# Performance work log

Measured on AMD Instinct MI355X. Metric: run time of the kernel, lower is better.

Reference implementation:

```python
import jax, jax.numpy as jnp
import numpy as np

B, T, D, H = 4, 2048, 1024, 16
HD = D // H  # 64
EPS = 1e-5

def _layernorm(x, g, b):
    mu = jnp.mean(x, axis=-1, keepdims=True)
    var = jnp.var(x, axis=-1, keepdims=True)
    return (x - mu) * jax.lax.rsqrt(var + EPS) * g + b

def setup_inputs() -> dict:
    key = jax.random.key(0)
    ks = jax.random.split(key, 8)
    s = D ** -0.5
    return {
        "x":  jax.random.normal(ks[0], (B, T, D), jnp.float32),
        "Wq": jax.random.normal(ks[1], (H, D, HD), jnp.float32) * s,
        "Wk": jax.random.normal(ks[2], (H, D, HD), jnp.float32) * s,
        "Wv": jax.random.normal(ks[3], (H, D, HD), jnp.float32) * s,
        "Wp": jax.random.normal(ks[4], (D, D), jnp.float32) * s,
        "bp": jnp.zeros((D,), jnp.float32),
        "W1": jax.random.normal(ks[5], (D, 4 * D), jnp.float32) * s,
        "b1": jnp.zeros((4 * D,), jnp.float32),
        "W2": jax.random.normal(ks[6], (4 * D, D), jnp.float32) * (4 * D) ** -0.5,
        "b2": jnp.zeros((D,), jnp.float32),
        "g1": jnp.ones((D,), jnp.float32),
        "be1": jnp.zeros((D,), jnp.float32),
        "g2": jnp.ones((D,), jnp.float32),
        "be2": jnp.zeros((D,), jnp.float32),
    }

def reference(x, Wq, Wk, Wv, Wp, bp, W1, b1, W2, b2, g1, be1, g2, be2):
    # --- pre-LN causal MHA (all heads batched; torch code loops per head) ---
    h = _layernorm(x, g1, be1)                       # [B,T,D]
    q = jnp.einsum('btd,hdk->bhtk', h, Wq)
    k = jnp.einsum('btd,hdk->bhtk', h, Wk)
    v = jnp.einsum('btd,hdk->bhtk', h, Wv)
    scores = jnp.einsum('bhtk,bhsk->bhts', q, k) * (HD ** -0.5)
    causal = jnp.tril(jnp.ones((T, T), bool))
    scores = jnp.where(causal, scores, -jnp.inf)
    w = jax.nn.softmax(scores, axis=-1)              # [B,H,T,T]
    o = jnp.einsum('bhts,bhsk->bhtk', w, v)          # [B,H,T,HD]
    o = o.transpose(0, 2, 1, 3).reshape(x.shape[0], x.shape[1], D)  # concat heads
    x = x + o @ Wp + bp                              # residual 1
    # --- pre-LN FFN ---
    h2 = _layernorm(x, g2, be2)
    ff = jax.nn.relu(h2 @ W1 + b1) @ W2 + b2
    return x + ff
```

## Files before the change

### kernel.cpp

```cpp
#include <hip/hip_runtime.h>
#include <hip/hip_bf16.h>
#include <math.h>

#define Bsz 4
#define Tsz 2048
#define Dsz 1024
#define Hn  16
#define HDs 64

typedef __attribute__((ext_vector_type(8))) short bf16x8;
typedef __attribute__((ext_vector_type(4))) float f32x4;

typedef const __attribute__((address_space(1))) void gvoid;
typedef __attribute__((address_space(3))) void lvoid;

__device__ __forceinline__ void async_copy16(const short* g, short* l) {
    __builtin_amdgcn_global_load_lds((gvoid*)g, (lvoid*)l, 16, 0, 0);
}

__device__ __forceinline__ short f2bf(float x) {
    __hip_bfloat16 h = __float2bfloat16(x);
    return *reinterpret_cast<short*>(&h);
}

__device__ __forceinline__ unsigned int pack_bf16(float hi, float lo) {
    unsigned int uh = __float_as_uint(hi) + 0x8000u;
    unsigned int ul = __float_as_uint(lo) + 0x8000u;
    return __builtin_amdgcn_perm(uh, ul, 0x07060302u);
}

__device__ __forceinline__ size_t headed_idx(int m, int c) {
    int b = m >> 11, t = m & 2047, h = c >> 6, kc = c & 63;
    return (((size_t)(b * Hn + h) * Tsz + t) << 6) + kc;
}

__global__ __launch_bounds__(256) void ln_kernel(const float* __restrict__ x,
                                                 const float* __restrict__ g,
                                                 const float* __restrict__ beta,
                                                 short* __restrict__ out)
{
    const int row = blockIdx.x;
    const float* xr = x + (size_t)row * Dsz;
    float v[4];
    float s = 0.f, s2 = 0.f;
#pragma unroll
    for (int i = 0; i < 4; ++i) {
        v[i] = xr[threadIdx.x + 256 * i];
        s += v[i];
        s2 += v[i] * v[i];
    }
#pragma unroll
    for (int off = 32; off; off >>= 1) {
        s  += __shfl_xor(s,  off);
        s2 += __shfl_xor(s2, off);
    }
    __shared__ float red[8];
    const int wave = threadIdx.x >> 6;
    if ((threadIdx.x & 63) == 0) { red[wave * 2] = s; red[wave * 2 + 1] = s2; }
    __syncthreads();
    s  = red[0] + red[2] + red[4] + red[6];
    s2 = red[1] + red[3] + red[5] + red[7];
    const float mu  = s * (1.f / Dsz);
    const float var = s2 * (1.f / Dsz) - mu * mu;
    const float rs  = rsqrtf(var + 1e-5f);
    short* orow = out + (size_t)row * Dsz;
#pragma unroll
    for (int i = 0; i < 4; ++i) {
        int col = threadIdx.x + 256 * i;
        orow[col] = f2bf((v[i] - mu) * rs * g[col] + beta[col]);
    }
}

__global__ __launch_bounds__(256) void transpose_cvt(
    const float* __restrict__ in, short* __restrict__ outp, int R, int C)
{
    __shared__ float tile[32][33];
    const int r0 = blockIdx.y * 32, c0 = blockIdx.x * 32;
    const size_t so = (size_t)blockIdx.z * R * C;
    const int tx = threadIdx.x & 31, ty = threadIdx.x >> 5;
    const float* ip = in + so;
    short* op = outp + so;
#pragma unroll
    for (int i = 0; i < 4; ++i)
        tile[ty + i * 8][tx] = ip[(size_t)(r0 + ty + i * 8) * C + c0 + tx];
    __syncthreads();
#pragma unroll
    for (int i = 0; i < 4; ++i)
        op[(size_t)(c0 + ty + i * 8) * R + r0 + tx] = f2bf(tile[tx][ty + i * 8]);
}

__global__ __launch_bounds__(256) void transpose_cvt_qkv(
    const float* __restrict__ Wq, const float* __restrict__ Wk,
    const float* __restrict__ Wv, short* __restrict__ outp)
{
    __shared__ float tile[32][33];
    const int z = blockIdx.z;
    const float* in = (z < 16) ? Wq : (z < 32) ? Wk : Wv;
    const int zz = z & 15;
    const int r0 = blockIdx.y * 32, c0 = blockIdx.x * 32;
    const int tx = threadIdx.x & 31, ty = threadIdx.x >> 5;
    const float* ip = in + (size_t)zz * (1024 * 64);
    short* op = outp + (size_t)z * (1024 * 64);
#pragma unroll
    for (int i = 0; i < 4; ++i)
        tile[ty + i * 8][tx] = ip[(size_t)(r0 + ty + i * 8) * 64 + c0 + tx];
    __syncthreads();
#pragma unroll
    for (int i = 0; i < 4; ++i)
        op[(size_t)(c0 + ty + i * 8) * 1024 + r0 + tx] = f2bf(tile[tx][ty + i * 8]);
}

template <int EPI>
__global__ __launch_bounds__(256) void gemm_mfma(
    const short* __restrict__ A, const short* __restrict__ Bt,
    const float* __restrict__ bias, const float* __restrict__ resid,
    float* __restrict__ Cf, short* __restrict__ Cb0,
    short* __restrict__ Cb1, short* __restrict__ Cb2,
    int M, int N, int K, float scale)
{
    __shared__ short As[128 * 32];
    __shared__ short Bs[128 * 32];
    const int tid  = threadIdx.x;
    const int lane = tid & 63, wave = tid >> 6;
    const int quad = lane >> 4, l16 = lane & 15;
    const int m0 = blockIdx.y * 128, n0 = blockIdx.x * 128;
    const int wm = (wave >> 1) * 64, wn = (wave & 1) * 64;

    f32x4 acc[4][4];
#pragma unroll
    for (int i = 0; i < 4; ++i)
#pragma unroll
        for (int j = 0; j < 4; ++j) acc[i][j] = f32x4{0.f, 0.f, 0.f, 0.f};

    const short* gA = A  + (size_t)(m0 + wave * 32 + (lane >> 2)) * K + (lane & 3) * 8;
    const short* gB = Bt + (size_t)(n0 + wave * 32 + (lane >> 2)) * K + (lane & 3) * 8;
    short* lA0 = As + wave * 1024;
    short* lA1 = As + wave * 1024 + 512;
    short* lB0 = Bs + wave * 1024;
    short* lB1 = Bs + wave * 1024 + 512;
    const size_t rstep = (size_t)16 * K;

    for (int k0 = 0; k0 < K; k0 += 32) {
        async_copy16(gA,         lA0);
        async_copy16(gA + rstep, lA1);
        async_copy16(gB,         lB0);
        async_copy16(gB + rstep, lB1);
        gA += 32; gB += 32;
        __syncthreads();
        bf16x8 af[4], bfr[4];
#pragma unroll
        for (int mt = 0; mt < 4; ++mt)
            af[mt] = *(const bf16x8*)(As + (wm + mt * 16 + l16) * 32 + quad * 8);
#pragma unroll
        for (int nt = 0; nt < 4; ++nt)
            bfr[nt] = *(const bf16x8*)(Bs + (wn + nt * 16 + l16) * 32 + quad * 8);
#pragma unroll
        for (int mt = 0; mt < 4; ++mt)
#pragma unroll
            for (int nt = 0; nt < 4; ++nt)
                acc[mt][nt] = __builtin_amdgcn_mfma_f32_16x16x32_bf16(
                    af[mt], bfr[nt], acc[mt][nt], 0, 0, 0);
        __syncthreads();
    }

#pragma unroll
    for (int mt = 0; mt < 4; ++mt) {
#pragma unroll
        for (int nt = 0; nt < 4; ++nt) {
#pragma unroll
            for (int r = 0; r < 4; ++r) {
                const int m = m0 + wm + mt * 16 + quad * 4 + r;
                const int c = n0 + wn + nt * 16 + l16;
                float val = acc[mt][nt][r];
                if (EPI == 0) {
                    const int sel = c >> 10, cl = c & 1023;
                    if (sel == 0)
                        Cb0[headed_idx(m, cl)] = f2bf(val * scale);
                    else if (sel == 1)
                        Cb1[headed_idx(m, cl)] = f2bf(val);
                    else {
                        int b = m >> 11, t = m & 2047;
                        size_t idx = ((((size_t)((b << 4) | (cl >> 6)) << 6) | (cl & 63)) << 11) | t;
                        Cb2[idx] = f2bf(val);
                    }
                } else if (EPI == 2) {
                    size_t idx = (size_t)m * N + c;
                    Cf[idx] = val + bias[c] + resid[idx];
                } else {
                    float v2 = val + bias[c];
                    Cb0[(size_t)m * N + c] = f2bf(v2 > 0.f ? v2 : 0.f);
                }
            }
        }
    }
}

__global__ __launch_bounds__(256) void fattn_kernel(
    const short* __restrict__ Q,
    const short* __restrict__ K,
    const short* __restrict__ VT,
    short* __restrict__ O)
{
    __shared__ short p_lds[4][2][16 * 64];
    const int lane = threadIdx.x & 63;
    const int wave = threadIdx.x >> 6;
    const int quad = lane >> 4;
    const int l16  = lane & 15;
    const int j    = blockIdx.x * 4 + wave;
    const int bb = blockIdx.y >> 4, hh = blockIdx.y & 15;
    const size_t bhoff = (size_t)blockIdx.y * (Tsz * HDs);
    const short* Qb = Q + bhoff;
    const short* Kb = K + bhoff;
    const short* Vb = VT + bhoff;

    short* pw[2] = { &p_lds[wave][0][0], &p_lds[wave][1][0] };
    const int rd0 = l16 * 64 + (((quad    ) ^ (l16 & 7)) << 3);
    const int rd1 = l16 * 64 + (((quad + 4) ^ (l16 & 7)) << 3);

    for (int ti = 0; ti < 2; ++ti) {
        const int q0w = (ti ? (63 - j) : j) * 32;

        bf16x8 bq[2][2];
#pragma unroll
        for (int mt = 0; mt < 2; ++mt) {
            const short* qp = Qb + (size_t)(q0w + mt * 16 + l16) * 64 + quad * 8;
            bq[mt][0] = *(const bf16x8*)qp;
            bq[mt][1] = *(const bf16x8*)(qp + 32);
        }

        f32x4 oaccT[2][4];
        float lacc[2] = {0.f, 0.f};
#pragma unroll
        for (int mt = 0; mt < 2; ++mt)
#pragma unroll
            for (int nt = 0; nt < 4; ++nt) oaccT[mt][nt] = f32x4{0.f, 0.f, 0.f, 0.f};

        const int nch = (q0w + 31) / 64 + 1;

        bf16x8 ak[4][2];
#pragma unroll
        for (int ct = 0; ct < 4; ++ct) {
            const short* kp = Kb + (size_t)(ct * 16 + l16) * 64 + quad * 8;
            ak[ct][0] = *(const bf16x8*)kp;
            ak[ct][1] = *(const bf16x8*)(kp + 32);
        }

        for (int c = 0; c < nch; ++c) {
            const int s0 = c * 64;
            bf16x8 av[4][2];
#pragma unroll
            for (int nt = 0; nt < 4; ++nt) {
                const short* vp = Vb + (size_t)(nt * 16 + l16) * Tsz + s0 + quad * 8;
                av[nt][0] = *(const bf16x8*)vp;
                av[nt][1] = *(const bf16x8*)(vp + 32);
            }
            bf16x8 nk[4][2];
            if (c + 1 < nch) {
#pragma unroll
                for (int ct = 0; ct < 4; ++ct) {
                    const short* kp = Kb + (size_t)(s0 + 64 + ct * 16 + l16) * 64 + quad * 8;
                    nk[ct][0] = *(const bf16x8*)kp;
                    nk[ct][1] = *(const bf16x8*)(kp + 32);
                }
            }
            f32x4 sfr[2][4];
#pragma unroll
            for (int mt = 0; mt < 2; ++mt)
#pragma unroll
                for (int ct = 0; ct < 4; ++ct) {
                    f32x4 cc = {0.f, 0.f, 0.f, 0.f};
                    cc = __builtin_amdgcn_mfma_f32_16x16x32_bf16(ak[ct][0], bq[mt][0], cc, 0, 0, 0);
                    cc = __builtin_amdgcn_mfma_f32_16x16x32_bf16(ak[ct][1], bq[mt][1], cc, 0, 0, 0);
                    sfr[mt][ct] = cc;
                }
            if (s0 + 63 > q0w) {
#pragma unroll
                for (int mt = 0; mt < 2; ++mt) {
                    const int qr = q0w + mt * 16 + l16;
#pragma unroll
                    for (int ct = 0; ct < 4; ++ct)
#pragma unroll
                        for (int r = 0; r < 4; ++r)
                            if (s0 + ct * 16 + quad * 4 + r > qr)
                                sfr[mt][ct][r] = -INFINITY;
                }
            }
#pragma unroll
            for (int mt = 0; mt < 2; ++mt) {
#pragma unroll
                for (int ct = 0; ct < 4; ++ct) {
                    float p0 = __builtin_exp2f(sfr[mt][ct][0]);
                    float p1 = __builtin_exp2f(sfr[mt][ct][1]);
                    float p2 = __builtin_exp2f(sfr[mt][ct][2]);
                    float p3 = __builtin_exp2f(sfr[mt][ct][3]);
                    lacc[mt] += (p0 + p1) + (p2 + p3);
                    uint2 pkv;
                    pkv.x = pack_bf16(p1, p0);
                    pkv.y = pack_bf16(p3, p2);
                    const int g = (2 * ct + (quad >> 1)) ^ (l16 & 7);
                    *(uint2*)(pw[mt] + l16 * 64 + (g << 3) + (quad & 1) * 4) = pkv;
                }
            }
            bf16x8 bp[2][2];
            bp[0][0] = *(const bf16x8*)(pw[0] + rd0);
            bp[0][1] = *(const bf16x8*)(pw[0] + rd1);
            bp[1][0] = *(const bf16x8*)(pw[1] + rd0);
            bp[1][1] = *(const bf16x8*)(pw[1] + rd1);
#pragma unroll
            for (int nt = 0; nt < 4; ++nt)
#pragma unroll
                for (int mt = 0; mt < 2; ++mt) {
                    oaccT[mt][nt] = __builtin_amdgcn_mfma_f32_16x16x32_bf16(av[nt][0], bp[mt][0], oaccT[mt][nt], 0, 0, 0);
                    oaccT[mt][nt] = __builtin_amdgcn_mfma_f32_16x16x32_bf16(av[nt][1], bp[mt][1], oaccT[mt][nt], 0, 0, 0);
                }
            if (c + 1 < nch) {
#pragma unroll
                for (int ct = 0; ct < 4; ++ct) {
                    ak[ct][0] = nk[ct][0];
                    ak[ct][1] = nk[ct][1];
                }
            }
        }
#pragma unroll
        for (int mt = 0; mt < 2; ++mt) {
            float ps = lacc[mt];
            ps += __shfl_xor(ps, 16);
            ps += __shfl_xor(ps, 32);
            const float inv = 1.f / ps;
            short* orow = O + (size_t)(bb * Tsz + q0w + mt * 16 + l16) * Dsz + hh * 64;
#pragma unroll
            for (int nt = 0; nt < 4; ++nt) {
                uint2 pkv;
                pkv.x = pack_bf16(oaccT[mt][nt][1] * inv, oaccT[mt][nt][0] * inv);
                pkv.y = pack_bf16(oaccT[mt][nt][3] * inv, oaccT[mt][nt][2] * inv);
                *(uint2*)(orow + nt * 16 + quad * 4) = pkv;
            }
        }
    }
}

extern "C" void kernel_launch(void* const* d_in, const int* in_sizes, int n_in,
                              void* d_out, int out_size, void* d_ws, size_t ws_size,
                              hipStream_t stream) {
    const float* x   = (const float*)d_in[0];
    const float* Wq  = (const float*)d_in[1];
    const float* Wk  = (const float*)d_in[2];
    const float* Wv  = (const float*)d_in[3];
    const float* Wp  = (const float*)d_in[4];
    const float* bp  = (const float*)d_in[5];
    const float* W1  = (const float*)d_in[6];
    const float* b1  = (const float*)d_in[7];
    const float* W2  = (const float*)d_in[8];
    const float* b2  = (const float*)d_in[9];
    const float* g1  = (const float*)d_in[10];
    const float* be1 = (const float*)d_in[11];
    const float* g2  = (const float*)d_in[12];
    const float* be2 = (const float*)d_in[13];
    float* out = (float*)d_out;
    char*  W   = (char*)d_ws;

    short* h1  = (short*)(W);
    short* ff1 = (short*)(W);
    short* qb  = (short*)(W + (16ull << 20));
    short* kb  = (short*)(W + (32ull << 20));
    short* vtb = (short*)(W + (48ull << 20));
    short* o   = (short*)(W + (64ull << 20));
    short* h2  = (short*)(W + (80ull << 20));
    short* wqt = (short*)(W + (96ull << 20));
    short* wpt = (short*)(W + (102ull << 20));
    short* w1t = (short*)(W + (104ull << 20));
    short* w2t = (short*)(W + (112ull << 20));

    const int M = Bsz * Tsz;
    const float qscale = 0.125f * 1.44269504f;

    transpose_cvt_qkv<<<dim3(2, 32, 48), 256, 0, stream>>>(Wq, Wk, Wv, wqt);
    transpose_cvt<<<dim3(32, 32, 1),  256, 0, stream>>>(Wp, wpt, 1024, 1024);
    transpose_cvt<<<dim3(128, 32, 1), 256, 0, stream>>>(W1, w1t, 1024, 4096);
    transpose_cvt<<<dim3(32, 128, 1), 256, 0, stream>>>(W2, w2t, 4096, 1024);

    ln_kernel<<<dim3(M), 256, 0, stream>>>(x, g1, be1, h1);

    gemm_mfma<0><<<dim3(24, 64), 256, 0, stream>>>(
        h1, wqt, nullptr, nullptr, nullptr, qb, kb, vtb, M, 3072, 1024, qscale);

    fattn_kernel<<<dim3(8, Bsz * Hn), 256, 0, stream>>>(qb, kb, vtb, o);

    gemm_mfma<2><<<dim3(8, 64), 256, 0, stream>>>(
        o, wpt, bp, x, out, nullptr, nullptr, nullptr, M, 1024, 1024, 1.f);

    ln_kernel<<<dim3(M), 256, 0, stream>>>(out, g2, be2, h2);

    gemm_mfma<3><<<dim3(32, 64), 256, 0, stream>>>(
        h2, w1t, b1, nullptr, nullptr, ff1, nullptr, nullptr, M, 4096, 1024, 1.f);

    gemm_mfma<2><<<dim3(8, 64), 256, 0, stream>>>(
        ff1, w2t, b2, out, out, nullptr, nullptr, nullptr, M, 1024, 4096, 1.f);
}
```

Measured before the change: 611.3 us.

## Split attention KV chunks across wave pairs and remap blocks per XCD

The attention grid grows from 8x64 to 32x64 blocks. Each block takes two query tiles, and each tile is handled by two waves that process alternating 64-key chunks. The partial output accumulators and row sums are then combined through LDS. Block indices are also remapped so that all blocks for a given batch-head land on the same XCD, which should improve L2 reuse of K and V. The intent is to shorten the per-wave serial chain and raise occupancy. The cost is extra LDS traffic and two block-wide barriers at the end.

```diff
diff --git a/kernel.cpp b/kernel.cpp
--- a/kernel.cpp
+++ b/kernel.cpp
@@ -202,13 +202,24 @@
     short* __restrict__ O)
 {
     __shared__ short p_lds[4][2][16 * 64];
+    __shared__ float lred[2][2][16];
     const int lane = threadIdx.x & 63;
     const int wave = threadIdx.x >> 6;
     const int quad = lane >> 4;
     const int l16  = lane & 15;
-    const int j    = blockIdx.x * 4 + wave;
-    const int bb = blockIdx.y >> 4, hh = blockIdx.y & 15;
-    const size_t bhoff = (size_t)blockIdx.y * (Tsz * HDs);
+
+    const int lin  = blockIdx.y * 32 + blockIdx.x;
+    const int xcd  = lin & 7;
+    const int slot = lin >> 3;
+    const int bh   = xcd * 8 + (slot >> 5);
+    const int bx   = slot & 31;
+
+    const int tile = (wave < 2) ? (62 - 2 * bx) : (63 - 2 * bx);
+    const int par  = wave & 1;
+    const int q0w  = tile * 32;
+
+    const int bb = bh >> 4, hh = bh & 15;
+    const size_t bhoff = (size_t)bh * (Tsz * HDs);
     const short* Qb = Q + bhoff;
     const short* Kb = K + bhoff;
     const short* Vb = VT + bhoff;
@@ -217,122 +228,144 @@
     const int rd0 = l16 * 64 + (((quad    ) ^ (l16 & 7)) << 3);
     const int rd1 = l16 * 64 + (((quad + 4) ^ (l16 & 7)) << 3);
 
-    for (int ti = 0; ti < 2; ++ti) {
-        const int q0w = (ti ? (63 - j) : j) * 32;
-
-        bf16x8 bq[2][2];
+    bf16x8 bq[2][2];
+#pragma unroll
+    for (int mt = 0; mt < 2; ++mt) {
+        const short* qp = Qb + (size_t)(q0w + mt * 16 + l16) * 64 + quad * 8;
+        bq[mt][0] = *(const bf16x8*)qp;
+        bq[mt][1] = *(const bf16x8*)(qp + 32);
+    }
+
+    f32x4 oaccT[2][4];
+    float lacc[2] = {0.f, 0.f};
+#pragma unroll
+    for (int mt = 0; mt < 2; ++mt)
+#pragma unroll
+        for (int nt = 0; nt < 4; ++nt) oaccT[mt][nt] = f32x4{0.f, 0.f, 0.f, 0.f};
+
+    const int nch = (q0w + 31) / 64 + 1;
+
+    bf16x8 ak[4][2];
+#pragma unroll
+    for (int ct = 0; ct < 4; ++ct) {
+        const short* kp = Kb + (size_t)(par * 64 + ct * 16 + l16) * 64 + quad * 8;
+        ak[ct][0] = *(const bf16x8*)kp;
+        ak[ct][1] = *(const bf16x8*)(kp + 32);
+    }
+
+    for (int c = par; c < nch; c += 2) {
+        const int s0 = c * 64;
+        bf16x8 av[4][2];
+#pragma unroll
+        for (int nt = 0; nt < 4; ++nt) {
+            const short* vp = Vb + (size_t)(nt * 16 + l16) * Tsz + s0 + quad * 8;
+            av[nt][0] = *(const bf16x8*)vp;
+            av[nt][1] = *(const bf16x8*)(vp + 32);
+        }
+        bf16x8 nk[4][2];
+        if (c + 2 < nch) {
+#pragma unroll
+            for (int ct = 0; ct < 4; ++ct) {
+                const short* kp = Kb + (size_t)(s0 + 128 + ct * 16 + l16) * 64 + quad * 8;
+                nk[ct][0] = *(const bf16x8*)kp;
+                nk[ct][1] = *(const bf16x8*)(kp + 32);
+            }
+        }
+        f32x4 sfr[2][4];
+#pragma unroll
+        for (int mt = 0; mt < 2; ++mt)
+#pragma unroll
+            for (int ct = 0; ct < 4; ++ct) {
+                f32x4 cc = {0.f, 0.f, 0.f, 0.f};
+                cc = __builtin_amdgcn_mfma_f32_16x16x32_bf16(ak[ct][0], bq[mt][0], cc, 0, 0, 0);
+                cc = __builtin_amdgcn_mfma_f32_16x16x32_bf16(ak[ct][1], bq[mt][1], cc, 0, 0, 0);
+                sfr[mt][ct] = cc;
+            }
+        if (s0 + 63 > q0w) {
+#pragma unroll
+            for (int mt = 0; mt < 2; ++mt) {
+                const int qr = q0w + mt * 16 + l16;
+#pragma unroll
+                for (int ct = 0; ct < 4; ++ct)
+#pragma unroll
+                    for (int r = 0; r < 4; ++r)
+                        if (s0 + ct * 16 + quad * 4 + r > qr)
+                            sfr[mt][ct][r] = -INFINITY;
+            }
+        }
 #pragma unroll
         for (int mt = 0; mt < 2; ++mt) {
-            const short* qp = Qb + (size_t)(q0w + mt * 16 + l16) * 64 + quad * 8;
-            bq[mt][0] = *(const bf16x8*)qp;
-            bq[mt][1] = *(const bf16x8*)(qp + 32);
-        }
-
-        f32x4 oaccT[2][4];
-        float lacc[2] = {0.f, 0.f};
-#pragma unroll
-        for (int mt = 0; mt < 2; ++mt)
-#pragma unroll
-            for (int nt = 0; nt < 4; ++nt) oaccT[mt][nt] = f32x4{0.f, 0.f, 0.f, 0.f};
-
-        const int nch = (q0w + 31) / 64 + 1;
-
-        bf16x8 ak[4][2];
-#pragma unroll
-        for (int ct = 0; ct < 4; ++ct) {
-            const short* kp = Kb + (size_t)(ct * 16 + l16) * 64 + quad * 8;
-            ak[ct][0] = *(const bf16x8*)kp;
-            ak[ct][1] = *(const bf16x8*)(kp + 32);
-        }
-
-        for (int c = 0; c < nch; ++c) {
-            const int s0 = c * 64;
-            bf16x8 av[4][2];
+#pragma unroll
+            for (int ct = 0; ct < 4; ++ct) {
+                float p0 = __builtin_exp2f(sfr[mt][ct][0]);
+                float p1 = __builtin_exp2f(sfr[mt][ct][1]);
+                float p2 = __builtin_exp2f(sfr[mt][ct][2]);
+                float p3 = __builtin_exp2f(sfr[mt][ct][3]);
+                lacc[mt] += (p0 + p1) + (p2 + p3);
+                uint2 pkv;
+                pkv.x = pack_bf16(p1, p0);
+                pkv.y = pack_bf16(p3, p2);
+                const int g = (2 * ct + (quad >> 1)) ^ (l16 & 7);
+                *(uint2*)(pw[mt] + l16 * 64 + (g << 3) + (quad & 1) * 4) = pkv;
+            }
+        }
+        bf16x8 bp[2][2];
+        bp[0][0] = *(const bf16x8*)(pw[0] + rd0);
+        bp[0][1] = *(const bf16x8*)(pw[0] + rd1);
+        bp[1][0] = *(const bf16x8*)(pw[1] + rd0);
+        bp[1][1] = *(const bf16x8*)(pw[1] + rd1);
+#pragma unroll
+        for (int nt = 0; nt < 4; ++nt)
+#pragma unroll
+            for (int mt = 0; mt < 2; ++mt) {
+                oaccT[mt][nt] = __builtin_amdgcn_mfma_f32_16x16x32_bf16(av[nt][0], bp[mt][0], oaccT[mt][nt], 0, 0, 0);
+                oaccT[mt][nt] = __builtin_amdgcn_mfma_f32_16x16x32_bf16(av[nt][1], bp[mt][1], oaccT[mt][nt], 0, 0, 0);
+            }
+        if (c + 2 < nch) {
+#pragma unroll
+            for (int ct = 0; ct < 4; ++ct) {
+                ak[ct][0] = nk[ct][0];
+                ak[ct][1] = nk[ct][1];
+            }
+        }
+    }
+
+    float ps[2];
+#pragma unroll
+    for (int mt = 0; mt < 2; ++mt) {
+        float v = lacc[mt];
+        v += __shfl_xor(v, 16);
+        v += __shfl_xor(v, 32);
+        ps[mt] = v;
+    }
+    __syncthreads();
+    float* buf = (float*)&p_lds[wave & ~1][0][0];
+    if (wave & 1) {
+#pragma unroll
+        for (int mt = 0; mt < 2; ++mt) {
+#pragma unroll
+            for (int nt = 0; nt < 4; ++nt)
+#pragma unroll
+                for (int r = 0; r < 4; ++r)
+                    buf[(mt * 16 + nt * 4 + r) * 64 + lane] = oaccT[mt][nt][r];
+            if (quad == 0) lred[wave >> 1][mt][l16] = ps[mt];
+        }
+    }
+    __syncthreads();
+    if (!(wave & 1)) {
+#pragma unroll
+        for (int mt = 0; mt < 2; ++mt) {
+            const float inv = 1.f / (ps[mt] + lred[wave >> 1][mt][l16]);
+            short* orow = O + (size_t)(bb * Tsz + q0w + mt * 16 + l16) * Dsz + hh * 64;
 #pragma unroll
             for (int nt = 0; nt < 4; ++nt) {
-                const short* vp = Vb + (size_t)(nt * 16 + l16) * Tsz + s0 + quad * 8;
-                av[nt][0] = *(const bf16x8*)vp;
-                av[nt][1] = *(const bf16x8*)(vp + 32);
-            }
-            bf16x8 nk[4][2];
-            if (c + 1 < nch) {
-#pragma unroll
-                for (int ct = 0; ct < 4; ++ct) {
-                    const short* kp = Kb + (size_t)(s0 + 64 + ct * 16 + l16) * 64 + quad * 8;
-                    nk[ct][0] = *(const bf16x8*)kp;
-                    nk[ct][1] = *(const bf16x8*)(kp + 32);
-                }
-            }
-            f32x4 sfr[2][4];
-#pragma unroll
-            for (int mt = 0; mt < 2; ++mt)
-#pragma unroll
-                for (int ct = 0; ct < 4; ++ct) {
-                    f32x4 cc = {0.f, 0.f, 0.f, 0.f};
-                    cc = __builtin_amdgcn_mfma_f32_16x16x32_bf16(ak[ct][0], bq[mt][0], cc, 0, 0, 0);
-                    cc = __builtin_amdgcn_mfma_f32_16x16x32_bf16(ak[ct][1], bq[mt][1], cc, 0, 0, 0);
-                    sfr[mt][ct] = cc;
-                }
-            if (s0 + 63 > q0w) {
-#pragma unroll
-                for (int mt = 0; mt < 2; ++mt) {
-                    const int qr = q0w + mt * 16 + l16;
-#pragma unroll
-                    for (int ct = 0; ct < 4; ++ct)
-#pragma unroll
-                        for (int r = 0; r < 4; ++r)
-                            if (s0 + ct * 16 + quad * 4 + r > qr)
-                                sfr[mt][ct][r] = -INFINITY;
-                }
-            }
-#pragma unroll
-            for (int mt = 0; mt < 2; ++mt) {
-#pragma unroll
-                for (int ct = 0; ct < 4; ++ct) {
-                    float p0 = __builtin_exp2f(sfr[mt][ct][0]);
-                    float p1 = __builtin_exp2f(sfr[mt][ct][1]);
-                    float p2 = __builtin_exp2f(sfr[mt][ct][2]);
-                    float p3 = __builtin_exp2f(sfr[mt][ct][3]);
-                    lacc[mt] += (p0 + p1) + (p2 + p3);
-                    uint2 pkv;
-                    pkv.x = pack_bf16(p1, p0);
-                    pkv.y = pack_bf16(p3, p2);
-                    const int g = (2 * ct + (quad >> 1)) ^ (l16 & 7);
-                    *(uint2*)(pw[mt] + l16 * 64 + (g << 3) + (quad & 1) * 4) = pkv;
-                }
-            }
-            bf16x8 bp[2][2];
-            bp[0][0] = *(const bf16x8*)(pw[0] + rd0);
-            bp[0][1] = *(const bf16x8*)(pw[0] + rd1);
-            bp[1][0] = *(const bf16x8*)(pw[1] + rd0);
-            bp[1][1] = *(const bf16x8*)(pw[1] + rd1);
-#pragma unroll
-            for (int nt = 0; nt < 4; ++nt)
-#pragma unroll
-                for (int mt = 0; mt < 2; ++mt) {
-                    oaccT[mt][nt] = __builtin_amdgcn_mfma_f32_16x16x32_bf16(av[nt][0], bp[mt][0], oaccT[mt][nt], 0, 0, 0);
-                    oaccT[mt][nt] = __builtin_amdgcn_mfma_f32_16x16x32_bf16(av[nt][1], bp[mt][1], oaccT[mt][nt], 0, 0, 0);
-                }
-            if (c + 1 < nch) {
-#pragma unroll
-                for (int ct = 0; ct < 4; ++ct) {
-                    ak[ct][0] = nk[ct][0];
-                    ak[ct][1] = nk[ct][1];
-                }
-            }
-        }
-#pragma unroll
-        for (int mt = 0; mt < 2; ++mt) {
-            float ps = lacc[mt];
-            ps += __shfl_xor(ps, 16);
-            ps += __shfl_xor(ps, 32);
-            const float inv = 1.f / ps;
-            short* orow = O + (size_t)(bb * Tsz + q0w + mt * 16 + l16) * Dsz + hh * 64;
-#pragma unroll
-            for (int nt = 0; nt < 4; ++nt) {
+                float o0 = (oaccT[mt][nt][0] + buf[(mt * 16 + nt * 4 + 0) * 64 + lane]) * inv;
+                float o1 = (oaccT[mt][nt][1] + buf[(mt * 16 + nt * 4 + 1) * 64 + lane]) * inv;
+                float o2 = (oaccT[mt][nt][2] + buf[(mt * 16 + nt * 4 + 2) * 64 + lane]) * inv;
+                float o3 = (oaccT[mt][nt][3] + buf[(mt * 16 + nt * 4 + 3) * 64 + lane]) * inv;
                 uint2 pkv;
-                pkv.x = pack_bf16(oaccT[mt][nt][1] * inv, oaccT[mt][nt][0] * inv);
-                pkv.y = pack_bf16(oaccT[mt][nt][3] * inv, oaccT[mt][nt][2] * inv);
+                pkv.x = pack_bf16(o1, o0);
+                pkv.y = pack_bf16(o3, o2);
                 *(uint2*)(orow + nt * 16 + quad * 4) = pkv;
             }
         }
@@ -384,7 +417,7 @@
     gemm_mfma<0><<<dim3(24, 64), 256, 0, stream>>>(
         h1, wqt, nullptr, nullptr, nullptr, qb, kb, vtb, M, 3072, 1024, qscale);
 
-    fattn_kernel<<<dim3(8, Bsz * Hn), 256, 0, stream>>>(qb, kb, vtb, o);
+    fattn_kernel<<<dim3(32, Bsz * Hn), 256, 0, stream>>>(qb, kb, vtb, o);
 
     gemm_mfma<2><<<dim3(8, 64), 256, 0, stream>>>(
         o, wpt, bp, x, out, nullptr, nullptr, nullptr, M, 1024, 1024, 1.f);
```

Result: slower. 635.7 us (+4.0%).

## Share K/V tiles across waves via double-buffered LDS async staging in attention

Applied to the files above, without the earlier changes.

The flash attention kernel now has the four waves of a block work on one contiguous 128-row query tile. K and V chunks are staged once per block into double-buffered, swizzled LDS with global_load_lds, instead of each wave loading them from global memory. The old per-wave pairing of front and back query tiles is replaced by a grid of 16 tiles launched largest-first, with launch_bounds raised to request 3 blocks. This cuts redundant global loads and overlaps the next chunk's fetch with compute. In exchange it adds block-wide barriers every chunk, and the waves within a block now have uneven causal work.

```diff
diff --git a/kernel.cpp b/kernel.cpp
--- a/kernel.cpp
+++ b/kernel.cpp
@@ -195,73 +195,88 @@
     }
 }
 
-__global__ __launch_bounds__(256) void fattn_kernel(
+__global__ __launch_bounds__(256, 3) void fattn_kernel(
     const short* __restrict__ Q,
     const short* __restrict__ K,
     const short* __restrict__ VT,
     short* __restrict__ O)
 {
+    __shared__ short Kl[2][64 * 64];
+    __shared__ short Vl[2][64 * 64];
     __shared__ short p_lds[4][2][16 * 64];
-    const int lane = threadIdx.x & 63;
-    const int wave = threadIdx.x >> 6;
-    const int quad = lane >> 4;
-    const int l16  = lane & 15;
-    const int j    = blockIdx.x * 4 + wave;
-    const int bb = blockIdx.y >> 4, hh = blockIdx.y & 15;
-    const size_t bhoff = (size_t)blockIdx.y * (Tsz * HDs);
+    const int tid  = threadIdx.x;
+    const int lane = tid & 63, wave = tid >> 6;
+    const int quad = lane >> 4, l16 = lane & 15;
+
+    const int tile = 15 - blockIdx.x;
+    const int q0   = tile * 128;
+    const int q0w  = q0 + wave * 32;
+    const int bh   = blockIdx.y;
+    const int bb = bh >> 4, hh = bh & 15;
+    const size_t bhoff = (size_t)bh * (Tsz * HDs);
     const short* Qb = Q + bhoff;
     const short* Kb = K + bhoff;
     const short* Vb = VT + bhoff;
 
+    const int s_a = tid, s_b = tid + 256;
+    const int ra = s_a >> 3, ga = (s_a & 7) ^ (ra & 7);
+    const int rb = s_b >> 3, gb = (s_b & 7) ^ (rb & 7);
+
     short* pw[2] = { &p_lds[wave][0][0], &p_lds[wave][1][0] };
     const int rd0 = l16 * 64 + (((quad    ) ^ (l16 & 7)) << 3);
     const int rd1 = l16 * 64 + (((quad + 4) ^ (l16 & 7)) << 3);
 
-    for (int ti = 0; ti < 2; ++ti) {
-        const int q0w = (ti ? (63 - j) : j) * 32;
-
-        bf16x8 bq[2][2];
-#pragma unroll
-        for (int mt = 0; mt < 2; ++mt) {
-            const short* qp = Qb + (size_t)(q0w + mt * 16 + l16) * 64 + quad * 8;
-            bq[mt][0] = *(const bf16x8*)qp;
-            bq[mt][1] = *(const bf16x8*)(qp + 32);
-        }
-
-        f32x4 oaccT[2][4];
-        float lacc[2] = {0.f, 0.f};
-#pragma unroll
-        for (int mt = 0; mt < 2; ++mt)
-#pragma unroll
-            for (int nt = 0; nt < 4; ++nt) oaccT[mt][nt] = f32x4{0.f, 0.f, 0.f, 0.f};
-
-        const int nch = (q0w + 31) / 64 + 1;
-
-        bf16x8 ak[4][2];
-#pragma unroll
-        for (int ct = 0; ct < 4; ++ct) {
-            const short* kp = Kb + (size_t)(ct * 16 + l16) * 64 + quad * 8;
-            ak[ct][0] = *(const bf16x8*)kp;
-            ak[ct][1] = *(const bf16x8*)(kp + 32);
-        }
-
-        for (int c = 0; c < nch; ++c) {
+    bf16x8 bq[2][2];
+#pragma unroll
+    for (int mt = 0; mt < 2; ++mt) {
+        const short* qp = Qb + (size_t)(q0w + mt * 16 + l16) * 64 + quad * 8;
+        bq[mt][0] = *(const bf16x8*)qp;
+        bq[mt][1] = *(const bf16x8*)(qp + 32);
+    }
+
+    f32x4 oaccT[2][4];
+    float lacc[2] = {0.f, 0.f};
+#pragma unroll
+    for (int mt = 0; mt < 2; ++mt)
+#pragma unroll
+        for (int nt = 0; nt < 4; ++nt) oaccT[mt][nt] = f32x4{0.f, 0.f, 0.f, 0.f};
+
+    const int nch  = (q0 + 127) / 64 + 1;
+    const int cmax = (q0w + 31) / 64;
+
+    auto stage = [&](int c, int buf) {
+        const int c64 = c * 64;
+        short* kb_l = &Kl[buf][0];
+        short* vb_l = &Vl[buf][0];
+        async_copy16(Kb + (((size_t)(c64 + ra)) << 6) + (ga << 3), kb_l + s_a * 8);
+        async_copy16(Kb + (((size_t)(c64 + rb)) << 6) + (gb << 3), kb_l + s_b * 8);
+        async_copy16(Vb + ((size_t)ra << 11) + c64 + (ga << 3), vb_l + s_a * 8);
+        async_copy16(Vb + ((size_t)rb << 11) + c64 + (gb << 3), vb_l + s_b * 8);
+    };
+
+    stage(0, 0);
+    __syncthreads();
+
+    for (int c = 0; c < nch; ++c) {
+        const int cur = c & 1;
+        if (c + 1 < nch) stage(c + 1, cur ^ 1);
+
+        if (c <= cmax) {
             const int s0 = c * 64;
-            bf16x8 av[4][2];
+            const short* Kc = &Kl[cur][0];
+            const short* Vc = &Vl[cur][0];
+            bf16x8 ak[4][2], av[4][2];
+#pragma unroll
+            for (int ct = 0; ct < 4; ++ct) {
+                const int r = ct * 16 + l16;
+                ak[ct][0] = *(const bf16x8*)(Kc + r * 64 + (((quad    ) ^ (r & 7)) << 3));
+                ak[ct][1] = *(const bf16x8*)(Kc + r * 64 + (((quad + 4) ^ (r & 7)) << 3));
+            }
 #pragma unroll
             for (int nt = 0; nt < 4; ++nt) {
-                const short* vp = Vb + (size_t)(nt * 16 + l16) * Tsz + s0 + quad * 8;
-                av[nt][0] = *(const bf16x8*)vp;
-                av[nt][1] = *(const bf16x8*)(vp + 32);
-            }
-            bf16x8 nk[4][2];
-            if (c + 1 < nch) {
-#pragma unroll
-                for (int ct = 0; ct < 4; ++ct) {
-                    const short* kp = Kb + (size_t)(s0 + 64 + ct * 16 + l16) * 64 + quad * 8;
-                    nk[ct][0] = *(const bf16x8*)kp;
-                    nk[ct][1] = *(const bf16x8*)(kp + 32);
-                }
+                const int r = nt * 16 + l16;
+                av[nt][0] = *(const bf16x8*)(Vc + r * 64 + (((quad    ) ^ (r & 7)) << 3));
+                av[nt][1] = *(const bf16x8*)(Vc + r * 64 + (((quad + 4) ^ (r & 7)) << 3));
             }
             f32x4 sfr[2][4];
 #pragma unroll
@@ -313,28 +328,23 @@
                     oaccT[mt][nt] = __builtin_amdgcn_mfma_f32_16x16x32_bf16(av[nt][0], bp[mt][0], oaccT[mt][nt], 0, 0, 0);
                     oaccT[mt][nt] = __builtin_amdgcn_mfma_f32_16x16x32_bf16(av[nt][1], bp[mt][1], oaccT[mt][nt], 0, 0, 0);
                 }
-            if (c + 1 < nch) {
-#pragma unroll
-                for (int ct = 0; ct < 4; ++ct) {
-                    ak[ct][0] = nk[ct][0];
-                    ak[ct][1] = nk[ct][1];
-                }
-            }
         }
-#pragma unroll
-        for (int mt = 0; mt < 2; ++mt) {
-            float ps = lacc[mt];
-            ps += __shfl_xor(ps, 16);
-            ps += __shfl_xor(ps, 32);
-            const float inv = 1.f / ps;
-            short* orow = O + (size_t)(bb * Tsz + q0w + mt * 16 + l16) * Dsz + hh * 64;
-#pragma unroll
-            for (int nt = 0; nt < 4; ++nt) {
-                uint2 pkv;
-                pkv.x = pack_bf16(oaccT[mt][nt][1] * inv, oaccT[mt][nt][0] * inv);
-                pkv.y = pack_bf16(oaccT[mt][nt][3] * inv, oaccT[mt][nt][2] * inv);
-                *(uint2*)(orow + nt * 16 + quad * 4) = pkv;
-            }
+        __syncthreads();
+    }
+
+#pragma unroll
+    for (int mt = 0; mt < 2; ++mt) {
+        float ps = lacc[mt];
+        ps += __shfl_xor(ps, 16);
+        ps += __shfl_xor(ps, 32);
+        const float inv = 1.f / ps;
+        short* orow = O + (size_t)(bb * Tsz + q0w + mt * 16 + l16) * Dsz + hh * 64;
+#pragma unroll
+        for (int nt = 0; nt < 4; ++nt) {
+            uint2 pkv;
+            pkv.x = pack_bf16(oaccT[mt][nt][1] * inv, oaccT[mt][nt][0] * inv);
+            pkv.y = pack_bf16(oaccT[mt][nt][3] * inv, oaccT[mt][nt][2] * inv);
+            *(uint2*)(orow + nt * 16 + quad * 4) = pkv;
         }
     }
 }
@@ -384,7 +394,7 @@
     gemm_mfma<0><<<dim3(24, 64), 256, 0, stream>>>(
         h1, wqt, nullptr, nullptr, nullptr, qb, kb, vtb, M, 3072, 1024, qscale);
 
-    fattn_kernel<<<dim3(8, Bsz * Hn), 256, 0, stream>>>(qb, kb, vtb, o);
+    fattn_kernel<<<dim3(16, Bsz * Hn), 256, 0, stream>>>(qb, kb, vtb, o);
 
     gemm_mfma<2><<<dim3(8, 64), 256, 0, stream>>>(
         o, wpt, bp, x, out, nullptr, nullptr, nullptr, M, 1024, 1024, 1.f);
```

New measurement: 596.6 us. 1.02x faster.
